# Kernel optimization log

Hardware: AMD Instinct MI355X
Metric: run time of the kernel (lower is better)

## Reference

```python
import jax, jax.numpy as jnp
import numpy as np

B, T, E, H = 2, 1024, 2048, 32
D = E // H
GROUP = (0.25, 0.25, 0.25, 0.25)
NEG = float(np.finfo(np.float32).min)


def quant_per_token(t, n_bits):
    # smoothquant-style: clamp(absmax, 1e-5) / qmax, per last-dim row
    qmax = 2 ** (n_bits - 1) - 1
    s = jnp.clip(jnp.abs(t).max(-1, keepdims=True), 1e-5, None) / qmax
    return jnp.round(t / s) * s


def w8a8_linear(x, W, b, quant_out=False):
    xq = quant_per_token(x, 8)           # per-token act quant
    Wq = quant_per_token(W, 8)           # per-output-channel weight quant (W: [out, in])
    y = xq @ Wq.T + b
    return quant_per_token(y, 8) if quant_out else y


def to_heads(x):
    # [B, T, E] -> [B*H, T, D]
    return x.reshape(B, T, H, D).transpose(0, 2, 1, 3).reshape(B * H, T, D)


def setup_inputs() -> dict:
    key = jax.random.key(0)
    ks = jax.random.split(key, 9)
    hidden_states = jax.random.normal(ks[0], (B, T, E), jnp.float32)
    causal = jnp.where(jnp.tril(jnp.ones((T, T), bool)), 0.0, NEG).astype(jnp.float32)
    attention_mask = jnp.broadcast_to(causal[None, None], (B, 1, T, T))
    w = 0.02
    return {
        'hidden_states': hidden_states,
        'attention_mask': attention_mask,
        'Wq': jax.random.normal(ks[1], (E, E), jnp.float32) * w,
        'bq': jax.random.normal(ks[2], (E,), jnp.float32) * w,
        'Wk': jax.random.normal(ks[3], (E, E), jnp.float32) * w,
        'bk': jax.random.normal(ks[4], (E,), jnp.float32) * w,
        'Wv': jax.random.normal(ks[5], (E, E), jnp.float32) * w,
        'bv': jax.random.normal(ks[6], (E,), jnp.float32) * w,
        'Wo': jax.random.normal(ks[7], (E, E), jnp.float32) * w,
        'bo': jax.random.normal(ks[8], (E,), jnp.float32) * w,
    }


def reference(hidden_states, attention_mask, Wq, bq, Wk, bk, Wv, bv, Wo, bo):
    scaling = D ** -0.5
    q = w8a8_linear(hidden_states, Wq, bq, quant_out=True) * scaling  # [B,T,E]
    k = w8a8_linear(hidden_states, Wk, bk)                            # [B,T,E]
    v = w8a8_linear(hidden_states, Wv, bv)                            # [B,T,E]

    # ---- heavy-hitter scoring pass (pre-4bit-quant K) ----
    q1, k1 = to_heads(q), to_heads(k)                                 # [BH,T,D]
    aw = jnp.einsum('btd,bsd->bts', q1, k1)                           # [BH,T,T]
    aw = aw.reshape(B, H, T, T) + attention_mask
    aw = jnp.maximum(aw, NEG).reshape(B * H, T, T)
    tmp_attn = jax.nn.softmax(aw, axis=-1)
    acc = tmp_attn.sum(axis=1).sum(axis=0)[None, :]                   # [1,T]
    row_vector = jnp.arange(T, 0, -1).astype(jnp.float32)[None, :]    # T, T-1, ..., 1
    acc = acc / row_vector / (B * H)

    # ---- group-wise top-k heavy-hitter selection ----
    range_size_or = int(T / len(GROUP) / 2)
    start = 1
    idx_list = []
    for i, ratio in enumerate(GROUP):
        rs = int(T * ratio)
        end = min(start + rs - 1, T) if i < len(GROUP) - 1 else T
        partial = acc[:, start - 1:end]
        _, ti = jax.lax.top_k(partial, range_size_or)
        idx_list.append(ti + start - 1)
        start = end + 1
    topk_idx = jnp.concatenate(idx_list, axis=-1).reshape(-1)

    # ---- mixed-precision K quantization ----
    k_abs = jnp.abs(k)
    # fake_quant_mix (8-bit): amax(...)[0] in torch indexes batch 0 -> scales [T,1]
    s_mix = jnp.clip(k_abs.max(-1, keepdims=True)[0] / 127.0, 1e-5, None)  # [T,1]
    k_imp = jnp.round(k / s_mix) * s_mix
    # fake_quant (4-bit, per-row): clamp then divide by 7
    s4 = jnp.clip(k_abs.max(-1, keepdims=True), 1e-5, None) / 7.0
    kq = jnp.round(k / s4) * s4
    kq = kq.at[:, topk_idx, :].set(k_imp[:, topk_idx, :])
    # fake_quant_v (4-bit, per-tensor)
    sv = jnp.clip(jnp.abs(v).max(), 1e-5, None) / 7.0
    vq = jnp.round(v / sv) * sv

    # ---- actual attention with quantized K/V ----
    q2, k2, v2 = to_heads(q), to_heads(kq), to_heads(vq)
    aw2 = jnp.einsum('btd,bsd->bts', q2, k2).reshape(B, H, T, T) + attention_mask
    aw2 = jnp.maximum(aw2, NEG).reshape(B * H, T, T)
    probs = jax.nn.softmax(aw2, axis=-1)
    out = jnp.einsum('bts,bsd->btd', probs, v2)                       # [BH,T,D]
    out = out.reshape(B, H, T, D).transpose(0, 2, 1, 3).reshape(B, T, E)
    return w8a8_linear(out, Wo, bo)
```

## Files before the change

kernel.cpp:

```cpp
#include <hip/hip_runtime.h>
#include <stdint.h>

#define NEG_INF (-__builtin_inff())
#define L2E 1.4426950408889634f

namespace {
constexpr int kT   = 1024;
constexpr int kE   = 2048;
}

using bf16x8 = __attribute__((ext_vector_type(8))) short;
using f32x4  = __attribute__((ext_vector_type(4))) float;
using i32x4  = __attribute__((ext_vector_type(4))) int;
using i32x16 = __attribute__((ext_vector_type(16))) int;

#define MFMA_BF16(a, b, c) __builtin_amdgcn_mfma_f32_16x16x32_bf16((a), (b), (c), 0, 0, 0)
#define MFMA_I8_32(a, b, c) __builtin_amdgcn_mfma_i32_32x32x32_i8((a), (b), (c), 0, 0, 0)

__device__ __forceinline__ void gload16(const void* g, void* l) {
  __builtin_amdgcn_global_load_lds((const __attribute__((address_space(1))) unsigned*)g,
                                   (__attribute__((address_space(3))) unsigned*)l, 16, 0, 0);
}
__device__ __forceinline__ unsigned bfr(float x) {
  unsigned u = __float_as_uint(x);
// ... 200 lines not shown
      q.z = (short)bfr(rintf(v.z / s));
      q.w = (short)bfr(rintf(v.w / s));
      *reinterpret_cast<short4*>(ki + (size_t)row * kE + i) = q;
    }
    if (tid == 0) skg[row] = s;
  } else {
    const int t = bid - 2048;
    const int tt = t & 15, bh = t >> 4;
    const int b = bh >> 5, h = bh & 31;
    const float sv = fmaxf(__uint_as_float(*vmax), 1e-5f) / 7.f;
    __shared__ short tr[64][80];
#pragma unroll
    for (int i = 0; i < 4; ++i) {
      const int e = i * 256 + tid;
      const int tok = e >> 4, d4 = (e & 15) * 4;
      const float4 v = *reinterpret_cast<const float4*>(
          &Vb[(size_t)(b * kT + tt * 64 + tok) * kE + h * 64 + d4]);
      tr[d4 + 0][tok] = (short)bfr(rintf(v.x / sv));
      tr[d4 + 1][tok] = (short)bfr(rintf(v.y / sv));
      tr[d4 + 2][tok] = (short)bfr(rintf(v.z / sv));
      tr[d4 + 3][tok] = (short)bfr(rintf(v.w / sv));
    }
    __syncthreads();
#pragma unroll
    for (int i = 0; i < 2; ++i) {
      const int e = i * 256 + tid;
      const int d = e >> 3, u = e & 7;
      const bf16x8 row = *reinterpret_cast<const bf16x8*>(&tr[d][u * 8]);
      *reinterpret_cast<bf16x8*>(&vt[(size_t)(bh * 64 + d) * kT + tt * 64 + u * 8]) = row;
    }
  }
}

__device__ __forceinline__ void gemm_i8_body(int m0, int n0,
                                             const int8_t* __restrict__ A,
                                             const float* __restrict__ sa,
                                             const int8_t* __restrict__ Bw,
                                             const float* __restrict__ sw,
                                             const float* __restrict__ bias,
                                             float* __restrict__ Y,
                                             int8_t* AsBase, int8_t* BsBase) {
  const int tid = threadIdx.x;
  const int lane = tid & 63, w = tid >> 6;
  const int l31 = lane & 31, lh = lane >> 5;
  const int wm = (w >> 1) * 64, wn = (w & 1) * 64;

  const i32x16 zero16 = {0};
  i32x16 acc00 = zero16, acc01 = zero16, acc10 = zero16, acc11 = zero16;

  auto stage = [&](int buf, int k0) {
    int8_t* As = AsBase + buf * 8192;
    int8_t* Bs = BsBase + buf * 8192;
#pragma unroll
    for (int i = 0; i < 2; ++i) {
      const int s = i * 256 + tid;
      const int row = s >> 2, gp = s & 3;
      const int gs = gp ^ ((row >> 1) & 3);
      gload16(A + (size_t)(m0 + row) * kE + k0 + gs * 16, As + s * 16);
    }
#pragma unroll
    for (int i = 0; i < 2; ++i) {
      const int s = i * 256 + tid;
      const int row = s >> 2, gp = s & 3;
      const int gs = gp ^ ((row >> 1) & 3);
      gload16(Bw + (size_t)(n0 + row) * kE + k0 + gs * 16, Bs + s * 16);
    }
  };

  stage(0, 0);
  __syncthreads();
  int cur = 0;

  const int ar0 = wm + l31, ar1 = wm + 32 + l31;
  const int br0 = wn + l31, br1 = wn + 32 + l31;
  const int sa0 = (ar0 >> 1) & 3, sa1 = (ar1 >> 1) & 3;
  const int sb0 = (br0 >> 1) & 3, sb1 = (br1 >> 1) & 3;

  for (int k0 = 0; k0 < kE; k0 += 64) {
    if (k0 + 64 < kE) stage(cur ^ 1, k0 + 64);
    const int8_t* As = AsBase + cur * 8192;
    const int8_t* Bs = BsBase + cur * 8192;
#pragma unroll
    for (int j = 0; j < 2; ++j) {
      const int gn = lh + 2 * j;
      const i32x4 a0 = *reinterpret_cast<const i32x4*>(As + ((ar0 << 2) + (gn ^ sa0)) * 16);
      const i32x4 a1 = *reinterpret_cast<const i32x4*>(As + ((ar1 << 2) + (gn ^ sa1)) * 16);
      const i32x4 b0 = *reinterpret_cast<const i32x4*>(Bs + ((br0 << 2) + (gn ^ sb0)) * 16);
      const i32x4 b1 = *reinterpret_cast<const i32x4*>(Bs + ((br1 << 2) + (gn ^ sb1)) * 16);
      acc00 = MFMA_I8_32(a0, b0, acc00);
      acc01 = MFMA_I8_32(a0, b1, acc01);
      acc10 = MFMA_I8_32(a1, b0, acc10);
      acc11 = MFMA_I8_32(a1, b1, acc11);
    }
    __syncthreads();
    cur ^= 1;
  }

#pragma unroll
  for (int fn = 0; fn < 2; ++fn) {
    const int col = n0 + wn + fn * 32 + l31;
    const float swn = sw[col], bn = bias[col];
#pragma unroll
    for (int fm = 0; fm < 2; ++fm) {
      const i32x16 accv = (fm == 0) ? ((fn == 0) ? acc00 : acc01)
                                    : ((fn == 0) ? acc10 : acc11);
      const int r0 = m0 + wm + fm * 32 + 4 * lh;
#pragma unroll
      for (int reg = 0; reg < 16; ++reg) {
        const int row = r0 + (reg & 3) + 8 * (reg >> 2);
        Y[(size_t)row * kE + col] = (float)accv[reg] * sa[row] * swn + bn;
      }
    }
  }
}

__global__ __launch_bounds__(256) void k_gemm_i8(const int8_t* __restrict__ A,
                                                 const float* __restrict__ sa,
                                                 const int8_t* __restrict__ Bw,
                                                 const float* __restrict__ sw,
                                                 const float* __restrict__ bias,
                                                 float* __restrict__ Y) {
  __shared__ int8_t As[2 * 8192];
  __shared__ int8_t Bs[2 * 8192];
  const int linear = blockIdx.x + (blockIdx.y << 4);
  const int nid = (linear & 7) * 32 + (linear >> 3);
  const int x = nid & 15, y = nid >> 4;
  gemm_i8_body(y * 128, x * 128, A, sa, Bw, sw, bias, Y, As, Bs);
}

__global__ __launch_bounds__(256) void k_gemm_qkv(const int8_t* __restrict__ A,
                                                  const float* __restrict__ sa,
                                                  const int8_t* __restrict__ Wq,
                                                  const int8_t* __restrict__ Wk,
                                                  const int8_t* __restrict__ Wv,
                                                  const float* __restrict__ sWall,
                                                  const float* __restrict__ bq,
                                                  const float* __restrict__ bk,
                                                  const float* __restrict__ bv,
                                                  float* __restrict__ qb,
                                                  float* __restrict__ kb,
                                                  float* __restrict__ vb) {
  __shared__ int8_t As[2 * 8192];
  __shared__ int8_t Bs[2 * 8192];
  const int linear = blockIdx.x + (blockIdx.y << 4) + (blockIdx.z << 8);
  const int nid = (linear & 7) * 96 + (linear >> 3);
  const int x = nid & 15, y = (nid >> 4) & 15, z = nid >> 8;
  const int8_t* Bw = (z == 0) ? Wq : (z == 1) ? Wk : Wv;
  const float* sw = sWall + (size_t)z * kE;
  const float* bias = (z == 0) ? bq : (z == 1) ? bk : bv;
  float* Y = (z == 0) ? qb : (z == 1) ? kb : vb;
  gemm_i8_body(y * 128, x * 128, A, sa, Bw, sw, bias, Y, As, Bs);
}

__global__ __launch_bounds__(256) void k_attn1(const short* __restrict__ qi,
                                               const short* __restrict__ khi,
                                               const short* __restrict__ klo,
                                               const float* __restrict__ sqg,
                                               float* __restrict__ accPart) {
  const int linear = blockIdx.x + (blockIdx.y << 3);
  const int nid = ((linear & 7) << 6) | (linear >> 3);
  const int r1 = nid & 7, r2 = 15 - r1, bh = nid >> 3;
  const int b = bh >> 5, h = bh & 31;
  const int tid = threadIdx.x, lane = tid & 63, w = tid >> 6;
  const int g = lane >> 4, c16 = lane & 15;
  const int swz = c16 & 7;

  __shared__ short qs1[64 * 64];
  __shared__ short qs2[64 * 64];
  __shared__ short hbuf[2][64 * 64];
  __shared__ short lbuf[2][64 * 64];
  __shared__ float accL[1024];
  __shared__ float Arow[128], Crow[128];

  for (int i = tid; i < 1024; i += 256) accL[i] = 0.f;

  const int st8 = tid >> 3, su = tid & 7;
  {
    const int tokb1 = b * kT + r1 * 64;
    const int tokb2 = b * kT + r2 * 64;
#pragma unroll
    for (int i = 0; i < 2; ++i) {
      const int tok = i * 32 + st8;
      const int co = ((su ^ (tok & 7)) << 3);
      gload16(qi + (size_t)(tokb1 + tok) * kE + h * 64 + co, &qs1[tok * 64 + su * 8]);
      gload16(qi + (size_t)(tokb2 + tok) * kE + h * 64 + co, &qs2[tok * 64 + su * 8]);
    }
  }
  auto stage = [&](int buf, int kt) {
    const int tokb = b * kT + kt * 64;
#pragma unroll
    for (int i = 0; i < 2; ++i) {
      const int tok = i * 32 + st8;
      const size_t gsrc = (size_t)(tokb + tok) * kE + h * 64 + ((su ^ (tok & 7)) << 3);
      gload16(khi + gsrc, &hbuf[buf][tok * 64 + su * 8]);
      gload16(klo + gsrc, &lbuf[buf][tok * 64 + su * 8]);
    }
  };

  stage(0, 0);
  __syncthreads();

  const int qrow = w * 16 + c16;
  const bf16x8 q1_0 = *reinterpret_cast<const bf16x8*>(&qs1[qrow * 64 + ((g ^ swz) << 3)]);
  const bf16x8 q1_1 = *reinterpret_cast<const bf16x8*>(&qs1[qrow * 64 + (((4 + g) ^ swz) << 3)]);
  const bf16x8 q2_0 = *reinterpret_cast<const bf16x8*>(&qs2[qrow * 64 + ((g ^ swz) << 3)]);
  const bf16x8 q2_1 = *reinterpret_cast<const bf16x8*>(&qs2[qrow * 64 + (((4 + g) ^ swz) << 3)]);
  const float A1c = sqg[b * kT + r1 * 64 + qrow] * L2E;
  const float A2c = sqg[b * kT + r2 * 64 + qrow] * L2E;

  float m1 = NEG_INF, l1 = 0.f, m2_ = NEG_INF, l2 = 0.f;
  int cur = 0;

  for (int kt = 0; kt <= r2; ++kt) {
    if (kt < r2) stage(cur ^ 1, kt + 1);
    const bool act1 = kt <= r1;
    float p1[4][4], p2[4][4];
    float pm1 = NEG_INF, pm2 = NEG_INF;
#pragma unroll
    for (int f = 0; f < 4; ++f) {
      const int tokl = f * 16 + c16;
      const bf16x8 ah0 = *reinterpret_cast<const bf16x8*>(&hbuf[cur][tokl * 64 + ((g ^ swz) << 3)]);
      const bf16x8 ah1 = *reinterpret_cast<const bf16x8*>(&hbuf[cur][tokl * 64 + (((4 + g) ^ swz) << 3)]);
      const bf16x8 al0 = *reinterpret_cast<const bf16x8*>(&lbuf[cur][tokl * 64 + ((g ^ swz) << 3)]);
      const bf16x8 al1 = *reinterpret_cast<const bf16x8*>(&lbuf[cur][tokl * 64 + (((4 + g) ^ swz) << 3)]);
      f32x4 sB = {0.f, 0.f, 0.f, 0.f};
      sB = MFMA_BF16(ah0, q2_0, sB);
      sB = MFMA_BF16(ah1, q2_1, sB);
      sB = MFMA_BF16(al0, q2_0, sB);
      sB = MFMA_BF16(al1, q2_1, sB);
      f32x4 sA = {0.f, 0.f, 0.f, 0.f};
      if (act1) {
        sA = MFMA_BF16(ah0, q1_0, sA);
        sA = MFMA_BF16(ah1, q1_1, sA);
        sA = MFMA_BF16(al0, q1_0, sA);
        sA = MFMA_BF16(al1, q1_1, sA);
      }
#pragma unroll
      for (int r = 0; r < 4; ++r) {
        const int tokd = f * 16 + g * 4 + r;
        float s2 = sB[r] * A2c;
        if (kt == r2 && tokd > qrow) s2 = NEG_INF;
        p2[f][r] = s2;
        pm2 = fmaxf(pm2, s2);
        float s1 = sA[r] * A1c;
        if (kt == r1 && tokd > qrow) s1 = NEG_INF;
        p1[f][r] = s1;
        pm1 = fmaxf(pm1, s1);
      }
    }
    {
      pm2 = fmaxf(pm2, __shfl_xor(pm2, 16));
      pm2 = fmaxf(pm2, __shfl_xor(pm2, 32));
      const bool upd = pm2 > m2_ + 8.f;
      const float mn = upd ? fmaxf(m2_, pm2) : m2_;
      const float fsc = fexp2(m2_ - mn);
      float rs = 0.f;
#pragma unroll
      for (int f = 0; f < 4; ++f)
#pragma unroll
        for (int r = 0; r < 4; ++r) rs += fexp2(p2[f][r] - mn);
      rs += __shfl_xor(rs, 16);
      rs += __shfl_xor(rs, 32);
      l2 = l2 * fsc + rs;
      m2_ = mn;
    }
    if (act1) {
      pm1 = fmaxf(pm1, __shfl_xor(pm1, 16));
      pm1 = fmaxf(pm1, __shfl_xor(pm1, 32));
      const bool upd = pm1 > m1 + 8.f;
      const float mn = upd ? fmaxf(m1, pm1) : m1;
      const float fsc = fexp2(m1 - mn);
      float rs = 0.f;
#pragma unroll
      for (int f = 0; f < 4; ++f)
#pragma unroll
        for (int r = 0; r < 4; ++r) rs += fexp2(p1[f][r] - mn);
      rs += __shfl_xor(rs, 16);
      rs += __shfl_xor(rs, 32);
      l1 = l1 * fsc + rs;
      m1 = mn;
    }
    __syncthreads();
    cur ^= 1;
  }

  if (g == 0) {
    Arow[qrow] = A1c;
    Crow[qrow] = -(m1 + __builtin_amdgcn_logf(l1));
    Arow[64 + qrow] = A2c;
    Crow[64 + qrow] = -(m2_ + __builtin_amdgcn_logf(l2));
  }
  stage(0, 0);
  __syncthreads();

  bf16x8 qa1_0[4], qa1_1[4], qa2_0[4], qa2_1[4];
  float Ar1[4][4], Cr1[4][4], Ar2[4][4], Cr2[4][4];
#pragma unroll
  for (int f = 0; f < 4; ++f) {
    const int qr = f * 16 + c16;
    qa1_0[f] = *reinterpret_cast<const bf16x8*>(&qs1[qr * 64 + ((g ^ swz) << 3)]);
    qa1_1[f] = *reinterpret_cast<const bf16x8*>(&qs1[qr * 64 + (((4 + g) ^ swz) << 3)]);
    qa2_0[f] = *reinterpret_cast<const bf16x8*>(&qs2[qr * 64 + ((g ^ swz) << 3)]);
    qa2_1[f] = *reinterpret_cast<const bf16x8*>(&qs2[qr * 64 + (((4 + g) ^ swz) << 3)]);
#pragma unroll
    for (int r = 0; r < 4; ++r) {
      const int tokd = f * 16 + g * 4 + r;
      Ar1[f][r] = Arow[tokd];
      Cr1[f][r] = Crow[tokd];
      Ar2[f][r] = Arow[64 + tokd];
      Cr2[f][r] = Crow[64 + tokd];
    }
  }

  const int ktokL = w * 16 + c16;
  cur = 0;
  for (int kt = 0; kt <= r2; ++kt) {
    if (kt < r2) stage(cur ^ 1, kt + 1);
    const bf16x8 kh0 = *reinterpret_cast<const bf16x8*>(&hbuf[cur][ktokL * 64 + ((g ^ swz) << 3)]);
    const bf16x8 kh1 = *reinterpret_cast<const bf16x8*>(&hbuf[cur][ktokL * 64 + (((4 + g) ^ swz) << 3)]);
    const bf16x8 kl0 = *reinterpret_cast<const bf16x8*>(&lbuf[cur][ktokL * 64 + ((g ^ swz) << 3)]);
    const bf16x8 kl1 = *reinterpret_cast<const bf16x8*>(&lbuf[cur][ktokL * 64 + (((4 + g) ^ swz) << 3)]);
    float csum = 0.f;
    if (kt < r2) {
#pragma unroll
      for (int f = 0; f < 4; ++f) {
        f32x4 sf = {0.f, 0.f, 0.f, 0.f};
        sf = MFMA_BF16(qa2_0[f], kh0, sf);
        sf = MFMA_BF16(qa2_1[f], kh1, sf);
        sf = MFMA_BF16(qa2_0[f], kl0, sf);
        sf = MFMA_BF16(qa2_1[f], kl1, sf);
#pragma unroll
        for (int r = 0; r < 4; ++r) csum += fexp2(fmaf(sf[r], Ar2[f][r], Cr2[f][r]));
      }
    } else {
#pragma unroll
      for (int f = 0; f < 4; ++f) {
        f32x4 sf = {0.f, 0.f, 0.f, 0.f};
        sf = MFMA_BF16(qa2_0[f], kh0, sf);
        sf = MFMA_BF16(qa2_1[f], kh1, sf);
        sf = MFMA_BF16(qa2_0[f], kl0, sf);
        sf = MFMA_BF16(qa2_1[f], kl1, sf);
#pragma unroll
        for (int r = 0; r < 4; ++r) {
          const float v = fexp2(fmaf(sf[r], Ar2[f][r], Cr2[f][r]));
          if (ktokL <= (f * 16 + g * 4 + r)) csum += v;
        }
      }
    }
    if (kt <= r1) {
      if (kt < r1) {
#pragma unroll
        for (int f = 0; f < 4; ++f) {
          f32x4 sf = {0.f, 0.f, 0.f, 0.f};
          sf = MFMA_BF16(qa1_0[f], kh0, sf);
          sf = MFMA_BF16(qa1_1[f], kh1, sf);
          sf = MFMA_BF16(qa1_0[f], kl0, sf);
          sf = MFMA_BF16(qa1_1[f], kl1, sf);
#pragma unroll
          for (int r = 0; r < 4; ++r) csum += fexp2(fmaf(sf[r], Ar1[f][r], Cr1[f][r]));
        }
      } else {
#pragma unroll
        for (int f = 0; f < 4; ++f) {
          f32x4 sf = {0.f, 0.f, 0.f, 0.f};
          sf = MFMA_BF16(qa1_0[f], kh0, sf);
          sf = MFMA_BF16(qa1_1[f], kh1, sf);
          sf = MFMA_BF16(qa1_0[f], kl0, sf);
          sf = MFMA_BF16(qa1_1[f], kl1, sf);
#pragma unroll
          for (int r = 0; r < 4; ++r) {
            const float v = fexp2(fmaf(sf[r], Ar1[f][r], Cr1[f][r]));
            if (ktokL <= (f * 16 + g * 4 + r)) csum += v;
          }
        }
      }
    }
    csum += __shfl_xor(csum, 16);
    csum += __shfl_xor(csum, 32);
    if (g == 0) accL[kt * 64 + ktokL] += csum;
    __syncthreads();
    cur ^= 1;
  }

  for (int i = tid; i < 1024; i += 256)
    accPart[(size_t)(bh * 8 + r1) * 1024 + i] = accL[i];
}

__global__ __launch_bounds__(1024) void k_acctopk(const float* __restrict__ part,
                                                  int* __restrict__ sel) {
  const int t = threadIdx.x;
  const int i = t & 255;
  const int sub = t >> 8;
  const int j = blockIdx.x * 256 + i;
  float s = 0.f;
  const int p0 = sub * 128;
  for (int p = p0; p < p0 + 128; ++p) s += part[(size_t)p * 1024 + j];
  __shared__ float partial[4][256];
  __shared__ float v[256];
  partial[sub][i] = s;
  __syncthreads();
  if (sub == 0) {
    const float tot = ((partial[0][i] + partial[1][i]) + partial[2][i]) + partial[3][i];
    v[i] = tot / (float)(kT - j) / 64.f;
  }
  __syncthreads();
  if (sub == 0) {
    const float vi = v[i];
    int rank = 0;
    for (int jj = 0; jj < 256; ++jj) {
      const float vj = v[jj];
      rank += (vj > vi) || (vj == vi && jj < i);
    }
    sel[j] = (rank < 128) ? 1 : 0;
  }
}

__global__ __launch_bounds__(256) void k_attn2(const short* __restrict__ qi,
                                               const short* __restrict__ ki,
                                               const short* __restrict__ vt,
                                               const float* __restrict__ sqg,
                                               const float* __restrict__ skg,
                                               const unsigned* __restrict__ vmax,
                                               float* __restrict__ ctx) {
  const int linear = blockIdx.x + (blockIdx.y << 3);
  const int nid = ((linear & 7) << 6) | (linear >> 3);
  const int r1 = nid & 7, r2 = 15 - r1, bh = nid >> 3;
  const int b = bh >> 5, h = bh & 31;
  const int tid = threadIdx.x, lane = tid & 63, w = tid >> 6;
  const int g = lane >> 4, c16 = lane & 15;
  const int swz = c16 & 7;
  const int wrow = w * 16 + c16;

  __shared__ short kbuf[2][64 * 64];
  __shared__ short vbuf[2][64 * 64];
  __shared__ float skl[2][64];

  const int qtokA = b * kT + r1 * 64 + wrow;
  const int qtokB = b * kT + r2 * 64 + wrow;
  bf16x8 qfA[2], qfB[2];
  qfA[0] = *reinterpret_cast<const bf16x8*>(qi + (size_t)qtokA * kE + h * 64 + g * 8);
  qfA[1] = *reinterpret_cast<const bf16x8*>(qi + (size_t)qtokA * kE + h * 64 + 32 + g * 8);
  qfB[0] = *reinterpret_cast<const bf16x8*>(qi + (size_t)qtokB * kE + h * 64 + g * 8);
  qfB[1] = *reinterpret_cast<const bf16x8*>(qi + (size_t)qtokB * kE + h * 64 + 32 + g * 8);
  const float sqA = sqg[qtokA] * L2E;
  const float sqB = sqg[qtokB] * L2E;
  const float sv = fmaxf(__uint_as_float(*vmax), 1e-5f) / 7.f;

  const int st8 = tid >> 3, su = tid & 7;
  auto stage = [&](int buf, int kt) {
    const int tokb = b * kT + kt * 64;
#pragma unroll
    for (int i = 0; i < 2; ++i) {
      const int tok = i * 32 + st8;
      gload16(ki + (size_t)(tokb + tok) * kE + h * 64 + ((su ^ (tok & 7)) << 3),
              &kbuf[buf][tok * 64 + su * 8]);
      gload16(vt + (size_t)(bh * 64 + tok) * kT + kt * 64 + ((su ^ (tok & 7)) << 3),
              &vbuf[buf][tok * 64 + su * 8]);
    }
    if (tid < 64) skl[buf][tid] = skg[tokb + tid];
  };

  float mA = NEG_INF, lA = 0.f, mB = NEG_INF, lB = 0.f;
  f32x4 otA[4], otB[4];
#pragma unroll
  for (int f = 0; f < 4; ++f) {
    otA[f] = (f32x4){0.f, 0.f, 0.f, 0.f};
    otB[f] = (f32x4){0.f, 0.f, 0.f, 0.f};
  }

  stage(0, 0);
  __syncthreads();
  int cur = 0;

  const int srcLo = c16 | ((g & 1) << 5);
  const int srcHi = srcLo | 16;
  const bool selq = ((g >> 1) & 1) != 0;

  for (int kt = 0; kt <= r2; ++kt) {
    if (kt < r2) stage(cur ^ 1, kt + 1);
    const bool act1 = kt <= r1;

    f32x4 sfB4[4], sfA4[4];
#pragma unroll
    for (int f = 0; f < 4; ++f) {
      const int tokl = f * 16 + c16;
      const bf16x8 k0 = *reinterpret_cast<const bf16x8*>(&kbuf[cur][tokl * 64 + ((g ^ swz) << 3)]);
      const bf16x8 k1 = *reinterpret_cast<const bf16x8*>(&kbuf[cur][tokl * 64 + (((4 + g) ^ swz) << 3)]);
      f32x4 s = {0.f, 0.f, 0.f, 0.f};
      s = MFMA_BF16(k0, qfB[0], s);
      s = MFMA_BF16(k1, qfB[1], s);
      sfB4[f] = s;
      f32x4 sa = {0.f, 0.f, 0.f, 0.f};
      if (act1) {
        sa = MFMA_BF16(k0, qfA[0], sa);
        sa = MFMA_BF16(k1, qfA[1], sa);
      }
      sfA4[f] = sa;
    }

    {
      float p[4][4];
      float pm = NEG_INF;
#pragma unroll
      for (int f = 0; f < 4; ++f)
#pragma unroll
        for (int r = 0; r < 4; ++r) {
          const int tokd = f * 16 + g * 4 + r;
          float s2 = sfB4[f][r] * skl[cur][tokd] * sqB;
          if (kt == r2 && tokd > wrow) s2 = NEG_INF;
          p[f][r] = s2;
          pm = fmaxf(pm, s2);
        }
      pm = fmaxf(pm, __shfl_xor(pm, 16));
      pm = fmaxf(pm, __shfl_xor(pm, 32));
      const bool upd = pm > mB + 8.f;
      const float mn = upd ? fmaxf(mB, pm) : mB;
      const float fsc = fexp2(mB - mn);
      mB = mn;
      float rs = 0.f;
#pragma unroll
      for (int f = 0; f < 4; ++f)
#pragma unroll
        for (int r = 0; r < 4; ++r) {
          const float e = fexp2(p[f][r] - mn);
          p[f][r] = e;
          rs += e;
        }
      rs += __shfl_xor(rs, 16);
      rs += __shfl_xor(rs, 32);
      lB = lB * fsc + rs;
      if (__any(upd)) {
#pragma unroll
        for (int f = 0; f < 4; ++f)
#pragma unroll
          for (int r = 0; r < 4; ++r) otB[f][r] *= fsc;
      }
#pragma unroll
      for (int c = 0; c < 2; ++c) {
        const unsigned q0a = pk2(p[2 * c][0], p[2 * c][1]);
        const unsigned q0b = pk2(p[2 * c][2], p[2 * c][3]);
        const unsigned q1a = pk2(p[2 * c + 1][0], p[2 * c + 1][1]);
        const unsigned q1b = pk2(p[2 * c + 1][2], p[2 * c + 1][3]);
        unsigned a0, a1;
        union { unsigned u[4]; bf16x8 v; } Bh;
        a0 = __shfl(q0a, srcLo); a1 = __shfl(q1a, srcLo); Bh.u[0] = selq ? a1 : a0;
        a0 = __shfl(q0b, srcLo); a1 = __shfl(q1b, srcLo); Bh.u[1] = selq ? a1 : a0;
        a0 = __shfl(q0a, srcHi); a1 = __shfl(q1a, srcHi); Bh.u[2] = selq ? a1 : a0;
        a0 = __shfl(q0b, srcHi); a1 = __shfl(q1b, srcHi); Bh.u[3] = selq ? a1 : a0;
#pragma unroll
        for (int fd = 0; fd < 4; ++fd) {
          const int d = fd * 16 + c16;
          const bf16x8 va = *reinterpret_cast<const bf16x8*>(
              &vbuf[cur][d * 64 + ((((c << 2) | g) ^ swz) << 3)]);
          otB[fd] = MFMA_BF16(va, Bh.v, otB[fd]);
        }
      }
    }

    if (act1) {
      float p[4][4];
      float pm = NEG_INF;
#pragma unroll
      for (int f = 0; f < 4; ++f)
#pragma unroll
        for (int r = 0; r < 4; ++r) {
          const int tokd = f * 16 + g * 4 + r;
          float s2 = sfA4[f][r] * skl[cur][tokd] * sqA;
          if (kt == r1 && tokd > wrow) s2 = NEG_INF;
          p[f][r] = s2;
          pm = fmaxf(pm, s2);
        }
      pm = fmaxf(pm, __shfl_xor(pm, 16));
      pm = fmaxf(pm, __shfl_xor(pm, 32));
      const bool upd = pm > mA + 8.f;
      const float mn = upd ? fmaxf(mA, pm) : mA;
      const float fsc = fexp2(mA - mn);
      mA = mn;
      float rs = 0.f;
#pragma unroll
      for (int f = 0; f < 4; ++f)
#pragma unroll
        for (int r = 0; r < 4; ++r) {
          const float e = fexp2(p[f][r] - mn);
          p[f][r] = e;
          rs += e;
        }
      rs += __shfl_xor(rs, 16);
      rs += __shfl_xor(rs, 32);
      lA = lA * fsc + rs;
      if (__any(upd)) {
#pragma unroll
        for (int f = 0; f < 4; ++f)
#pragma unroll
          for (int r = 0; r < 4; ++r) otA[f][r] *= fsc;
      }
#pragma unroll
      for (int c = 0; c < 2; ++c) {
        const unsigned q0a = pk2(p[2 * c][0], p[2 * c][1]);
        const unsigned q0b = pk2(p[2 * c][2], p[2 * c][3]);
        const unsigned q1a = pk2(p[2 * c + 1][0], p[2 * c + 1][1]);
        const unsigned q1b = pk2(p[2 * c + 1][2], p[2 * c + 1][3]);
        unsigned a0, a1;
        union { unsigned u[4]; bf16x8 v; } Bh;
        a0 = __shfl(q0a, srcLo); a1 = __shfl(q1a, srcLo); Bh.u[0] = selq ? a1 : a0;
        a0 = __shfl(q0b, srcLo); a1 = __shfl(q1b, srcLo); Bh.u[1] = selq ? a1 : a0;
        a0 = __shfl(q0a, srcHi); a1 = __shfl(q1a, srcHi); Bh.u[2] = selq ? a1 : a0;
        a0 = __shfl(q0b, srcHi); a1 = __shfl(q1b, srcHi); Bh.u[3] = selq ? a1 : a0;
#pragma unroll
        for (int fd = 0; fd < 4; ++fd) {
          const int d = fd * 16 + c16;
          const bf16x8 va = *reinterpret_cast<const bf16x8*>(
              &vbuf[cur][d * 64 + ((((c << 2) | g) ^ swz) << 3)]);
          otA[fd] = MFMA_BF16(va, Bh.v, otA[fd]);
        }
      }
    }

    __syncthreads();
    cur ^= 1;
  }

  const float ilA = sv / lA;
  const float ilB = sv / lB;
#pragma unroll
  for (int fd = 0; fd < 4; ++fd) {
    float4 oA, oB;
    oA.x = otA[fd][0] * ilA; oA.y = otA[fd][1] * ilA;
    oA.z = otA[fd][2] * ilA; oA.w = otA[fd][3] * ilA;
    oB.x = otB[fd][0] * ilB; oB.y = otB[fd][1] * ilB;
    oB.z = otB[fd][2] * ilB; oB.w = otB[fd][3] * ilB;
    *reinterpret_cast<float4*>(&ctx[(size_t)qtokA * kE + h * 64 + fd * 16 + g * 4]) = oA;
    *reinterpret_cast<float4*>(&ctx[(size_t)qtokB * kE + h * 64 + fd * 16 + g * 4]) = oB;
  }
}

extern "C" void kernel_launch(void* const* d_in, const int* in_sizes, int n_in,
                              void* d_out, int out_size, void* d_ws, size_t ws_size,
                              hipStream_t stream) {
  (void)in_sizes; (void)n_in; (void)out_size; (void)ws_size;
  const float* hs = (const float*)d_in[0];
  const float* Wq = (const float*)d_in[2];
  const float* bq = (const float*)d_in[3];
  const float* Wk = (const float*)d_in[4];
  const float* bk = (const float*)d_in[5];
  const float* Wv = (const float*)d_in[6];
  const float* bv = (const float*)d_in[7];
  const float* Wo = (const float*)d_in[8];
  const float* bo = (const float*)d_in[9];
  float* out = (float*)d_out;

  char* p = (char*)d_ws;
  auto take = [&](size_t bytes) {
    char* r = p;
    p += (bytes + 255) & ~(size_t)255;
    return r;
  };
  float* qb  = (float*)take((size_t)2048 * 2048 * 4);
  float* kb  = (float*)take((size_t)2048 * 2048 * 4);
  float* vb  = (float*)take((size_t)2048 * 2048 * 4);
  float* ctx = (float*)take((size_t)2048 * 2048 * 4);
  short* qiB = (short*)take((size_t)2048 * 2048 * 2);
  int8_t* xq  = (int8_t*)take((size_t)2048 * 2048);
  int8_t* woq = (int8_t*)take((size_t)2048 * 2048);
  float* sX    = (float*)take(2048 * 4);
  float* sWall = (float*)take(4 * 2048 * 4);
  float* sC    = (float*)take(2048 * 4);
  float* s4v   = (float*)take(2048 * 4);
  float* smix  = (float*)take(1024 * 4);
  int*   sel   = (int*)take(1024 * 4);
  float* sqg   = (float*)take(2048 * 4);
  float* skg   = (float*)take(2048 * 4);
  unsigned* vmax = (unsigned*)take(256);

  short* khi = (short*)qb;
  short* klo = (short*)qb + (size_t)2048 * 2048;
  short* kint = khi;
  short* vtp  = klo;
  float* accPart = ctx;
  int8_t* wqq = (int8_t*)ctx + ((size_t)2 << 20);
  int8_t* wkq = (int8_t*)ctx + ((size_t)6 << 20);
  int8_t* wvq = (int8_t*)ctx + ((size_t)10 << 20);
  int8_t* cq = xq;

  k_rowquant_all<<<dim3(2048, 5), 256, 0, stream>>>(hs, Wq, Wk, Wv, Wo,
                                                    xq, wqq, wkq, wvq, woq,
                                                    sX, sWall, vmax);

  k_gemm_qkv<<<dim3(16, 16, 3), 256, 0, stream>>>(xq, sX, wqq, wkq, wvq, sWall,
                                                  bq, bk, bv, qb, kb, vb);

  k_prep<<<2048, 256, 0, stream>>>(qb, kb, vb, qiB, sqg, khi, klo, s4v, smix, vmax);

  k_attn1<<<dim3(8, 64), 256, 0, stream>>>(qiB, khi, klo, sqg, accPart);
  k_acctopk<<<4, 1024, 0, stream>>>(accPart, sel);

  k_kvint<<<3072, 256, 0, stream>>>(kb, s4v, smix, sel, kint, skg, vb, vmax, vtp);

  k_attn2<<<dim3(8, 64), 256, 0, stream>>>(qiB, kint, vtp, sqg, skg, vmax, ctx);

  k_rowquant_i8<<<2048, 256, 0, stream>>>(ctx, cq, sC);
  k_gemm_i8<<<dim3(16, 16), 256, 0, stream>>>(cq, sC, woq, sWall + 3 * 2048, bo, out);
}
```

Before: 218.2 us.

## Split paired query tiles across separate waves in both attention kernels

Both attention kernels previously had each 4-wave block process two query tiles (r1 and r2) serially within the same waves. They now launch 512 threads, and waves 0-3 handle tile r1 while waves 4-7 handle tile r2, sharing the staged K/V buffers. Scoring-pass accumulators are kept per tile and summed at the end. This doubles in-flight wavefronts and shortens per-wave dependency chains. The cost is idle waves on the short tile once its range ends, plus higher register and LDS pressure per block.

Result: no change. 216.1 us (median of 3 runs) (-0.9%).

```diff
diff --git a/kernel.cpp b/kernel.cpp
--- a/kernel.cpp
+++ b/kernel.cpp
@@ -376,7 +376,7 @@
   gemm_i8_body(y * 128, x * 128, A, sa, Bw, sw, bias, Y, As, Bs);
 }
 
-__global__ __launch_bounds__(256) void k_attn1(const short* __restrict__ qi,
+__global__ __launch_bounds__(512) void k_attn1(const short* __restrict__ qi,
                                                const short* __restrict__ khi,
                                                const short* __restrict__ klo,
                                                const float* __restrict__ sqg,
@@ -388,226 +388,155 @@
   const int tid = threadIdx.x, lane = tid & 63, w = tid >> 6;
   const int g = lane >> 4, c16 = lane & 15;
   const int swz = c16 & 7;
-
-  __shared__ short qs1[64 * 64];
-  __shared__ short qs2[64 * 64];
+  const int myT = w >> 2, wl = w & 3;
+  const int myr = myT ? r2 : r1;
+
+  __shared__ short qs[2][64 * 64];
   __shared__ short hbuf[2][64 * 64];
   __shared__ short lbuf[2][64 * 64];
-  __shared__ float accL[1024];
+  __shared__ float accT[2][1024];
   __shared__ float Arow[128], Crow[128];
 
-  for (int i = tid; i < 1024; i += 256) accL[i] = 0.f;
+  for (int i = tid; i < 2048; i += 512) ((float*)accT)[i] = 0.f;
 
   const int st8 = tid >> 3, su = tid & 7;
   {
-    const int tokb1 = b * kT + r1 * 64;
-    const int tokb2 = b * kT + r2 * 64;
-#pragma unroll
-    for (int i = 0; i < 2; ++i) {
-      const int tok = i * 32 + st8;
-      const int co = ((su ^ (tok & 7)) << 3);
-      gload16(qi + (size_t)(tokb1 + tok) * kE + h * 64 + co, &qs1[tok * 64 + su * 8]);
-      gload16(qi + (size_t)(tokb2 + tok) * kE + h * 64 + co, &qs2[tok * 64 + su * 8]);
-    }
+    const int co = ((su ^ (st8 & 7)) << 3);
+    gload16(qi + (size_t)(b * kT + r1 * 64 + st8) * kE + h * 64 + co, &qs[0][st8 * 64 + su * 8]);
+    gload16(qi + (size_t)(b * kT + r2 * 64 + st8) * kE + h * 64 + co, &qs[1][st8 * 64 + su * 8]);
   }
   auto stage = [&](int buf, int kt) {
     const int tokb = b * kT + kt * 64;
-#pragma unroll
-    for (int i = 0; i < 2; ++i) {
-      const int tok = i * 32 + st8;
-      const size_t gsrc = (size_t)(tokb + tok) * kE + h * 64 + ((su ^ (tok & 7)) << 3);
-      gload16(khi + gsrc, &hbuf[buf][tok * 64 + su * 8]);
-      gload16(klo + gsrc, &lbuf[buf][tok * 64 + su * 8]);
-    }
+    const size_t gsrc = (size_t)(tokb + st8) * kE + h * 64 + ((su ^ (st8 & 7)) << 3);
+    gload16(khi + gsrc, &hbuf[buf][st8 * 64 + su * 8]);
+    gload16(klo + gsrc, &lbuf[buf][st8 * 64 + su * 8]);
   };
 
   stage(0, 0);
   __syncthreads();
 
-  const int qrow = w * 16 + c16;
-  const bf16x8 q1_0 = *reinterpret_cast<const bf16x8*>(&qs1[qrow * 64 + ((g ^ swz) << 3)]);
-  const bf16x8 q1_1 = *reinterpret_cast<const bf16x8*>(&qs1[qrow * 64 + (((4 + g) ^ swz) << 3)]);
-  const bf16x8 q2_0 = *reinterpret_cast<const bf16x8*>(&qs2[qrow * 64 + ((g ^ swz) << 3)]);
-  const bf16x8 q2_1 = *reinterpret_cast<const bf16x8*>(&qs2[qrow * 64 + (((4 + g) ^ swz) << 3)]);
-  const float A1c = sqg[b * kT + r1 * 64 + qrow] * L2E;
-  const float A2c = sqg[b * kT + r2 * 64 + qrow] * L2E;
-
-  float m1 = NEG_INF, l1 = 0.f, m2_ = NEG_INF, l2 = 0.f;
+  const int qrow = wl * 16 + c16;
+  const short* qsp = qs[myT];
+  const bf16x8 qf0 = *reinterpret_cast<const bf16x8*>(&qsp[qrow * 64 + ((g ^ swz) << 3)]);
+  const bf16x8 qf1 = *reinterpret_cast<const bf16x8*>(&qsp[qrow * 64 + (((4 + g) ^ swz) << 3)]);
+  const float Ac = sqg[b * kT + myr * 64 + qrow] * L2E;
+
+  float m = NEG_INF, l = 0.f;
   int cur = 0;
 
   for (int kt = 0; kt <= r2; ++kt) {
     if (kt < r2) stage(cur ^ 1, kt + 1);
-    const bool act1 = kt <= r1;
-    float p1[4][4], p2[4][4];
-    float pm1 = NEG_INF, pm2 = NEG_INF;
-#pragma unroll
-    for (int f = 0; f < 4; ++f) {
-      const int tokl = f * 16 + c16;
-      const bf16x8 ah0 = *reinterpret_cast<const bf16x8*>(&hbuf[cur][tokl * 64 + ((g ^ swz) << 3)]);
-      const bf16x8 ah1 = *reinterpret_cast<const bf16x8*>(&hbuf[cur][tokl * 64 + (((4 + g) ^ swz) << 3)]);
-      const bf16x8 al0 = *reinterpret_cast<const bf16x8*>(&lbuf[cur][tokl * 64 + ((g ^ swz) << 3)]);
-      const bf16x8 al1 = *reinterpret_cast<const bf16x8*>(&lbuf[cur][tokl * 64 + (((4 + g) ^ swz) << 3)]);
-      f32x4 sB = {0.f, 0.f, 0.f, 0.f};
-      sB = MFMA_BF16(ah0, q2_0, sB);
-      sB = MFMA_BF16(ah1, q2_1, sB);
-      sB = MFMA_BF16(al0, q2_0, sB);
-      sB = MFMA_BF16(al1, q2_1, sB);
-      f32x4 sA = {0.f, 0.f, 0.f, 0.f};
-      if (act1) {
-        sA = MFMA_BF16(ah0, q1_0, sA);
-        sA = MFMA_BF16(ah1, q1_1, sA);
-        sA = MFMA_BF16(al0, q1_0, sA);
-        sA = MFMA_BF16(al1, q1_1, sA);
+    if (kt <= myr) {
+      float p[4][4];
+      float pm = NEG_INF;
+#pragma unroll
+      for (int f = 0; f < 4; ++f) {
+        const int tokl = f * 16 + c16;
+        const bf16x8 ah0 = *reinterpret_cast<const bf16x8*>(&hbuf[cur][tokl * 64 + ((g ^ swz) << 3)]);
+        const bf16x8 ah1 = *reinterpret_cast<const bf16x8*>(&hbuf[cur][tokl * 64 + (((4 + g) ^ swz) << 3)]);
+        const bf16x8 al0 = *reinterpret_cast<const bf16x8*>(&lbuf[cur][tokl * 64 + ((g ^ swz) << 3)]);
+        const bf16x8 al1 = *reinterpret_cast<const bf16x8*>(&lbuf[cur][tokl * 64 + (((4 + g) ^ swz) << 3)]);
+        f32x4 sf = {0.f, 0.f, 0.f, 0.f};
+        sf = MFMA_BF16(ah0, qf0, sf);
+        sf = MFMA_BF16(ah1, qf1, sf);
+        sf = MFMA_BF16(al0, qf0, sf);
+        sf = MFMA_BF16(al1, qf1, sf);
+#pragma unroll
+        for (int r = 0; r < 4; ++r) {
+          const int tokd = f * 16 + g * 4 + r;
+          float s2 = sf[r] * Ac;
+          if (kt == myr && tokd > qrow) s2 = NEG_INF;
+          p[f][r] = s2;
+          pm = fmaxf(pm, s2);
+        }
       }
-#pragma unroll
-      for (int r = 0; r < 4; ++r) {
-        const int tokd = f * 16 + g * 4 + r;
-        float s2 = sB[r] * A2c;
-        if (kt == r2 && tokd > qrow) s2 = NEG_INF;
-        p2[f][r] = s2;
-        pm2 = fmaxf(pm2, s2);
-        float s1 = sA[r] * A1c;
-        if (kt == r1 && tokd > qrow) s1 = NEG_INF;
-        p1[f][r] = s1;
-        pm1 = fmaxf(pm1, s1);
-      }
-    }
-    {
-      pm2 = fmaxf(pm2, __shfl_xor(pm2, 16));
-      pm2 = fmaxf(pm2, __shfl_xor(pm2, 32));
-      const bool upd = pm2 > m2_ + 8.f;
-      const float mn = upd ? fmaxf(m2_, pm2) : m2_;
-      const float fsc = fexp2(m2_ - mn);
+      pm = fmaxf(pm, __shfl_xor(pm, 16));
+      pm = fmaxf(pm, __shfl_xor(pm, 32));
+      const bool upd = pm > m + 8.f;
+      const float mn = upd ? fmaxf(m, pm) : m;
+      const float fsc = fexp2(m - mn);
       float rs = 0.f;
 #pragma unroll
       for (int f = 0; f < 4; ++f)
 #pragma unroll
-        for (int r = 0; r < 4; ++r) rs += fexp2(p2[f][r] - mn);
+        for (int r = 0; r < 4; ++r) rs += fexp2(p[f][r] - mn);
       rs += __shfl_xor(rs, 16);
       rs += __shfl_xor(rs, 32);
-      l2 = l2 * fsc + rs;
-      m2_ = mn;
-    }
-    if (act1) {
-      pm1 = fmaxf(pm1, __shfl_xor(pm1, 16));
-      pm1 = fmaxf(pm1, __shfl_xor(pm1, 32));
-      const bool upd = pm1 > m1 + 8.f;
-      const float mn = upd ? fmaxf(m1, pm1) : m1;
-      const float fsc = fexp2(m1 - mn);
-      float rs = 0.f;
-#pragma unroll
-      for (int f = 0; f < 4; ++f)
-#pragma unroll
-        for (int r = 0; r < 4; ++r) rs += fexp2(p1[f][r] - mn);
-      rs += __shfl_xor(rs, 16);
-      rs += __shfl_xor(rs, 32);
-      l1 = l1 * fsc + rs;
-      m1 = mn;
+      l = l * fsc + rs;
+      m = mn;
     }
     __syncthreads();
     cur ^= 1;
   }
 
   if (g == 0) {
-    Arow[qrow] = A1c;
-    Crow[qrow] = -(m1 + __builtin_amdgcn_logf(l1));
-    Arow[64 + qrow] = A2c;
-    Crow[64 + qrow] = -(m2_ + __builtin_amdgcn_logf(l2));
+    Arow[myT * 64 + qrow] = Ac;
+    Crow[myT * 64 + qrow] = -(m + __builtin_amdgcn_logf(l));
   }
   stage(0, 0);
   __syncthreads();
 
-  bf16x8 qa1_0[4], qa1_1[4], qa2_0[4], qa2_1[4];
-  float Ar1[4][4], Cr1[4][4], Ar2[4][4], Cr2[4][4];
+  bf16x8 qa0[4], qa1[4];
+  float Ar[4][4], Cr[4][4];
 #pragma unroll
   for (int f = 0; f < 4; ++f) {
     const int qr = f * 16 + c16;
-    qa1_0[f] = *reinterpret_cast<const bf16x8*>(&qs1[qr * 64 + ((g ^ swz) << 3)]);
-    qa1_1[f] = *reinterpret_cast<const bf16x8*>(&qs1[qr * 64 + (((4 + g) ^ swz) << 3)]);
-    qa2_0[f] = *reinterpret_cast<const bf16x8*>(&qs2[qr * 64 + ((g ^ swz) << 3)]);
-    qa2_1[f] = *reinterpret_cast<const bf16x8*>(&qs2[qr * 64 + (((4 + g) ^ swz) << 3)]);
+    qa0[f] = *reinterpret_cast<const bf16x8*>(&qsp[qr * 64 + ((g ^ swz) << 3)]);
+    qa1[f] = *reinterpret_cast<const bf16x8*>(&qsp[qr * 64 + (((4 + g) ^ swz) << 3)]);
 #pragma unroll
     for (int r = 0; r < 4; ++r) {
-      const int tokd = f * 16 + g * 4 + r;
-      Ar1[f][r] = Arow[tokd];
-      Cr1[f][r] = Crow[tokd];
-      Ar2[f][r] = Arow[64 + tokd];
-      Cr2[f][r] = Crow[64 + tokd];
-    }
-  }
-
-  const int ktokL = w * 16 + c16;
+      const int tokd = myT * 64 + f * 16 + g * 4 + r;
+      Ar[f][r] = Arow[tokd];
+      Cr[f][r] = Crow[tokd];
+    }
+  }
+
+  const int ktokL = wl * 16 + c16;
   cur = 0;
   for (int kt = 0; kt <= r2; ++kt) {
     if (kt < r2) stage(cur ^ 1, kt + 1);
-    const bf16x8 kh0 = *reinterpret_cast<const bf16x8*>(&hbuf[cur][ktokL * 64 + ((g ^ swz) << 3)]);
-    const bf16x8 kh1 = *reinterpret_cast<const bf16x8*>(&hbuf[cur][ktokL * 64 + (((4 + g) ^ swz) << 3)]);
-    const bf16x8 kl0 = *reinterpret_cast<const bf16x8*>(&lbuf[cur][ktokL * 64 + ((g ^ swz) << 3)]);
-    const bf16x8 kl1 = *reinterpret_cast<const bf16x8*>(&lbuf[cur][ktokL * 64 + (((4 + g) ^ swz) << 3)]);
-    float csum = 0.f;
-    if (kt < r2) {
-#pragma unroll
-      for (int f = 0; f < 4; ++f) {
-        f32x4 sf = {0.f, 0.f, 0.f, 0.f};
-        sf = MFMA_BF16(qa2_0[f], kh0, sf);
-        sf = MFMA_BF16(qa2_1[f], kh1, sf);
-        sf = MFMA_BF16(qa2_0[f], kl0, sf);
-        sf = MFMA_BF16(qa2_1[f], kl1, sf);
-#pragma unroll
-        for (int r = 0; r < 4; ++r) csum += fexp2(fmaf(sf[r], Ar2[f][r], Cr2[f][r]));
-      }
-    } else {
-#pragma unroll
-      for (int f = 0; f < 4; ++f) {
-        f32x4 sf = {0.f, 0.f, 0.f, 0.f};
-        sf = MFMA_BF16(qa2_0[f], kh0, sf);
-        sf = MFMA_BF16(qa2_1[f], kh1, sf);
-        sf = MFMA_BF16(qa2_0[f], kl0, sf);
-        sf = MFMA_BF16(qa2_1[f], kl1, sf);
-#pragma unroll
-        for (int r = 0; r < 4; ++r) {
-          const float v = fexp2(fmaf(sf[r], Ar2[f][r], Cr2[f][r]));
-          if (ktokL <= (f * 16 + g * 4 + r)) csum += v;
-        }
-      }
-    }
-    if (kt <= r1) {
-      if (kt < r1) {
+    if (kt <= myr) {
+      const bf16x8 kh0 = *reinterpret_cast<const bf16x8*>(&hbuf[cur][ktokL * 64 + ((g ^ swz) << 3)]);
+      const bf16x8 kh1 = *reinterpret_cast<const bf16x8*>(&hbuf[cur][ktokL * 64 + (((4 + g) ^ swz) << 3)]);
+      const bf16x8 kl0 = *reinterpret_cast<const bf16x8*>(&lbuf[cur][ktokL * 64 + ((g ^ swz) << 3)]);
+      const bf16x8 kl1 = *reinterpret_cast<const bf16x8*>(&lbuf[cur][ktokL * 64 + (((4 + g) ^ swz) << 3)]);
+      float csum = 0.f;
+      if (kt < myr) {
 #pragma unroll
         for (int f = 0; f < 4; ++f) {
           f32x4 sf = {0.f, 0.f, 0.f, 0.f};
-          sf = MFMA_BF16(qa1_0[f], kh0, sf);
-          sf = MFMA_BF16(qa1_1[f], kh1, sf);
-          sf = MFMA_BF16(qa1_0[f], kl0, sf);
-          sf = MFMA_BF16(qa1_1[f], kl1, sf);
-#pragma unroll
-          for (int r = 0; r < 4; ++r) csum += fexp2(fmaf(sf[r], Ar1[f][r], Cr1[f][r]));
+          sf = MFMA_BF16(qa0[f], kh0, sf);
+          sf = MFMA_BF16(qa1[f], kh1, sf);
+          sf = MFMA_BF16(qa0[f], kl0, sf);
+          sf = MFMA_BF16(qa1[f], kl1, sf);
+#pragma unroll
+          for (int r = 0; r < 4; ++r) csum += fexp2(fmaf(sf[r], Ar[f][r], Cr[f][r]));
         }
       } else {
 #pragma unroll
         for (int f = 0; f < 4; ++f) {
           f32x4 sf = {0.f, 0.f, 0.f, 0.f};
-          sf = MFMA_BF16(qa1_0[f], kh0, sf);
-          sf = MFMA_BF16(qa1_1[f], kh1, sf);
-          sf = MFMA_BF16(qa1_0[f], kl0, sf);
-          sf = MFMA_BF16(qa1_1[f], kl1, sf);
+          sf = MFMA_BF16(qa0[f], kh0, sf);
+          sf = MFMA_BF16(qa1[f], kh1, sf);
+          sf = MFMA_BF16(qa0[f], kl0, sf);
+          sf = MFMA_BF16(qa1[f], kl1, sf);
 #pragma unroll
           for (int r = 0; r < 4; ++r) {
-            const float v = fexp2(fmaf(sf[r], Ar1[f][r], Cr1[f][r]));
+            const float v = fexp2(fmaf(sf[r], Ar[f][r], Cr[f][r]));
             if (ktokL <= (f * 16 + g * 4 + r)) csum += v;
           }
         }
       }
-    }
-    csum += __shfl_xor(csum, 16);
-    csum += __shfl_xor(csum, 32);
-    if (g == 0) accL[kt * 64 + ktokL] += csum;
+      csum += __shfl_xor(csum, 16);
+      csum += __shfl_xor(csum, 32);
+      if (g == 0) accT[myT][kt * 64 + ktokL] += csum;
+    }
     __syncthreads();
     cur ^= 1;
   }
 
-  for (int i = tid; i < 1024; i += 256)
-    accPart[(size_t)(bh * 8 + r1) * 1024 + i] = accL[i];
+  for (int i = tid; i < 1024; i += 512)
+    accPart[(size_t)(bh * 8 + r1) * 1024 + i] = accT[0][i] + accT[1][i];
 }
 
 __global__ __launch_bounds__(1024) void k_acctopk(const float* __restrict__ part,
@@ -639,7 +568,7 @@
   }
 }
 
-__global__ __launch_bounds__(256) void k_attn2(const short* __restrict__ qi,
+__global__ __launch_bounds__(512) void k_attn2(const short* __restrict__ qi,
                                                const short* __restrict__ ki,
                                                const short* __restrict__ vt,
                                                const float* __restrict__ sqg,
@@ -653,44 +582,35 @@
   const int tid = threadIdx.x, lane = tid & 63, w = tid >> 6;
   const int g = lane >> 4, c16 = lane & 15;
   const int swz = c16 & 7;
-  const int wrow = w * 16 + c16;
+  const int myT = w >> 2, wl = w & 3;
+  const int myr = myT ? r2 : r1;
+  const int wrow = wl * 16 + c16;
 
   __shared__ short kbuf[2][64 * 64];
   __shared__ short vbuf[2][64 * 64];
   __shared__ float skl[2][64];
 
-  const int qtokA = b * kT + r1 * 64 + wrow;
-  const int qtokB = b * kT + r2 * 64 + wrow;
-  bf16x8 qfA[2], qfB[2];
-  qfA[0] = *reinterpret_cast<const bf16x8*>(qi + (size_t)qtokA * kE + h * 64 + g * 8);
-  qfA[1] = *reinterpret_cast<const bf16x8*>(qi + (size_t)qtokA * kE + h * 64 + 32 + g * 8);
-  qfB[0] = *reinterpret_cast<const bf16x8*>(qi + (size_t)qtokB * kE + h * 64 + g * 8);
-  qfB[1] = *reinterpret_cast<const bf16x8*>(qi + (size_t)qtokB * kE + h * 64 + 32 + g * 8);
-  const float sqA = sqg[qtokA] * L2E;
-  const float sqB = sqg[qtokB] * L2E;
+  const int qtok = b * kT + myr * 64 + wrow;
+  bf16x8 qf[2];
+  qf[0] = *reinterpret_cast<const bf16x8*>(qi + (size_t)qtok * kE + h * 64 + g * 8);
+  qf[1] = *reinterpret_cast<const bf16x8*>(qi + (size_t)qtok * kE + h * 64 + 32 + g * 8);
+  const float sq2 = sqg[qtok] * L2E;
   const float sv = fmaxf(__uint_as_float(*vmax), 1e-5f) / 7.f;
 
   const int st8 = tid >> 3, su = tid & 7;
   auto stage = [&](int buf, int kt) {
     const int tokb = b * kT + kt * 64;
-#pragma unroll
-    for (int i = 0; i < 2; ++i) {
-      const int tok = i * 32 + st8;
-      gload16(ki + (size_t)(tokb + tok) * kE + h * 64 + ((su ^ (tok & 7)) << 3),
-              &kbuf[buf][tok * 64 + su * 8]);
-      gload16(vt + (size_t)(bh * 64 + tok) * kT + kt * 64 + ((su ^ (tok & 7)) << 3),
-              &vbuf[buf][tok * 64 + su * 8]);
-    }
+    gload16(ki + (size_t)(tokb + st8) * kE + h * 64 + ((su ^ (st8 & 7)) << 3),
+            &kbuf[buf][st8 * 64 + su * 8]);
+    gload16(vt + (size_t)(bh * 64 + st8) * kT + kt * 64 + ((su ^ (st8 & 7)) << 3),
+            &vbuf[buf][st8 * 64 + su * 8]);
     if (tid < 64) skl[buf][tid] = skg[tokb + tid];
   };
 
-  float mA = NEG_INF, lA = 0.f, mB = NEG_INF, lB = 0.f;
-  f32x4 otA[4], otB[4];
-#pragma unroll
-  for (int f = 0; f < 4; ++f) {
-    otA[f] = (f32x4){0.f, 0.f, 0.f, 0.f};
-    otB[f] = (f32x4){0.f, 0.f, 0.f, 0.f};
-  }
+  float m = NEG_INF, l = 0.f;
+  f32x4 ot[4];
+#pragma unroll
+  for (int f = 0; f < 4; ++f) ot[f] = (f32x4){0.f, 0.f, 0.f, 0.f};
 
   stage(0, 0);
   __syncthreads();
@@ -702,27 +622,19 @@
 
   for (int kt = 0; kt <= r2; ++kt) {
     if (kt < r2) stage(cur ^ 1, kt + 1);
-    const bool act1 = kt <= r1;
-
-    f32x4 sfB4[4], sfA4[4];
-#pragma unroll
-    for (int f = 0; f < 4; ++f) {
-      const int tokl = f * 16 + c16;
-      const bf16x8 k0 = *reinterpret_cast<const bf16x8*>(&kbuf[cur][tokl * 64 + ((g ^ swz) << 3)]);
-      const bf16x8 k1 = *reinterpret_cast<const bf16x8*>(&kbuf[cur][tokl * 64 + (((4 + g) ^ swz) << 3)]);
-      f32x4 s = {0.f, 0.f, 0.f, 0.f};
-      s = MFMA_BF16(k0, qfB[0], s);
-      s = MFMA_BF16(k1, qfB[1], s);
-      sfB4[f] = s;
-      f32x4 sa = {0.f, 0.f, 0.f, 0.f};
-      if (act1) {
-        sa = MFMA_BF16(k0, qfA[0], sa);
-        sa = MFMA_BF16(k1, qfA[1], sa);
+    if (kt <= myr) {
+      f32x4 sf4[4];
+#pragma unroll
+      for (int f = 0; f < 4; ++f) {
+        const int tokl = f * 16 + c16;
+        const bf16x8 k0 = *reinterpret_cast<const bf16x8*>(&kbuf[cur][tokl * 64 + ((g ^ swz) << 3)]);
+        const bf16x8 k1 = *reinterpret_cast<const bf16x8*>(&kbuf[cur][tokl * 64 + (((4 + g) ^ swz) << 3)]);
+        f32x4 s = {0.f, 0.f, 0.f, 0.f};
+        s = MFMA_BF16(k0, qf[0], s);
+        s = MFMA_BF16(k1, qf[1], s);
+        sf4[f] = s;
       }
-      sfA4[f] = sa;
-    }
-
-    {
+
       float p[4][4];
       float pm = NEG_INF;
 #pragma unroll
@@ -730,17 +642,17 @@
 #pragma unroll
         for (int r = 0; r < 4; ++r) {
           const int tokd = f * 16 + g * 4 + r;
-          float s2 = sfB4[f][r] * skl[cur][tokd] * sqB;
-          if (kt == r2 && tokd > wrow) s2 = NEG_INF;
+          float s2 = sf4[f][r] * skl[cur][tokd] * sq2;
+          if (kt == myr && tokd > wrow) s2 = NEG_INF;
           p[f][r] = s2;
           pm = fmaxf(pm, s2);
         }
       pm = fmaxf(pm, __shfl_xor(pm, 16));
       pm = fmaxf(pm, __shfl_xor(pm, 32));
-      const bool upd = pm > mB + 8.f;
-      const float mn = upd ? fmaxf(mB, pm) : mB;
-      const float fsc = fexp2(mB - mn);
-      mB = mn;
+      const bool upd = pm > m + 8.f;
+      const float mn = upd ? fmaxf(m, pm) : m;
+      const float fsc = fexp2(m - mn);
+      m = mn;
       float rs = 0.f;
 #pragma unroll
       for (int f = 0; f < 4; ++f)
@@ -752,12 +664,12 @@
         }
       rs += __shfl_xor(rs, 16);
       rs += __shfl_xor(rs, 32);
-      lB = lB * fsc + rs;
+      l = l * fsc + rs;
       if (__any(upd)) {
 #pragma unroll
         for (int f = 0; f < 4; ++f)
 #pragma unroll
-          for (int r = 0; r < 4; ++r) otB[f][r] *= fsc;
+          for (int r = 0; r < 4; ++r) ot[f][r] *= fsc;
       }
 #pragma unroll
       for (int c = 0; c < 2; ++c) {
@@ -776,85 +688,23 @@
           const int d = fd * 16 + c16;
           const bf16x8 va = *reinterpret_cast<const bf16x8*>(
               &vbuf[cur][d * 64 + ((((c << 2) | g) ^ swz) << 3)]);
-          otB[fd] = MFMA_BF16(va, Bh.v, otB[fd]);
+          ot[fd] = MFMA_BF16(va, Bh.v, ot[fd]);
         }
       }
     }
-
-    if (act1) {
-      float p[4][4];
-      float pm = NEG_INF;
-#pragma unroll
-      for (int f = 0; f < 4; ++f)
-#pragma unroll
-        for (int r = 0; r < 4; ++r) {
-          const int tokd = f * 16 + g * 4 + r;
-          float s2 = sfA4[f][r] * skl[cur][tokd] * sqA;
-          if (kt == r1 && tokd > wrow) s2 = NEG_INF;
-          p[f][r] = s2;
-          pm = fmaxf(pm, s2);
-        }
-      pm = fmaxf(pm, __shfl_xor(pm, 16));
-      pm = fmaxf(pm, __shfl_xor(pm, 32));
-      const bool upd = pm > mA + 8.f;
-      const float mn = upd ? fmaxf(mA, pm) : mA;
-      const float fsc = fexp2(mA - mn);
-      mA = mn;
-      float rs = 0.f;
-#pragma unroll
-      for (int f = 0; f < 4; ++f)
-#pragma unroll
-        for (int r = 0; r < 4; ++r) {
-          const float e = fexp2(p[f][r] - mn);
-          p[f][r] = e;
-          rs += e;
-        }
-      rs += __shfl_xor(rs, 16);
-      rs += __shfl_xor(rs, 32);
-      lA = lA * fsc + rs;
-      if (__any(upd)) {
-#pragma unroll
-        for (int f = 0; f < 4; ++f)
-#pragma unroll
-          for (int r = 0; r < 4; ++r) otA[f][r] *= fsc;
-      }
-#pragma unroll
-      for (int c = 0; c < 2; ++c) {
-        const unsigned q0a = pk2(p[2 * c][0], p[2 * c][1]);
-        const unsigned q0b = pk2(p[2 * c][2], p[2 * c][3]);
-        const unsigned q1a = pk2(p[2 * c + 1][0], p[2 * c + 1][1]);
-        const unsigned q1b = pk2(p[2 * c + 1][2], p[2 * c + 1][3]);
-        unsigned a0, a1;
-        union { unsigned u[4]; bf16x8 v; } Bh;
-        a0 = __shfl(q0a, srcLo); a1 = __shfl(q1a, srcLo); Bh.u[0] = selq ? a1 : a0;
-        a0 = __shfl(q0b, srcLo); a1 = __shfl(q1b, srcLo); Bh.u[1] = selq ? a1 : a0;
-        a0 = __shfl(q0a, srcHi); a1 = __shfl(q1a, srcHi); Bh.u[2] = selq ? a1 : a0;
-        a0 = __shfl(q0b, srcHi); a1 = __shfl(q1b, srcHi); Bh.u[3] = selq ? a1 : a0;
-#pragma unroll
-        for (int fd = 0; fd < 4; ++fd) {
-          const int d = fd * 16 + c16;
-          const bf16x8 va = *reinterpret_cast<const bf16x8*>(
-              &vbuf[cur][d * 64 + ((((c << 2) | g) ^ swz) << 3)]);
-          otA[fd] = MFMA_BF16(va, Bh.v, otA[fd]);
-        }
-      }
-    }
-
     __syncthreads();
     cur ^= 1;
   }
 
-  const float ilA = sv / lA;
-  const float ilB = sv / lB;
+  const float il = sv / l;
 #pragma unroll
   for (int fd = 0; fd < 4; ++fd) {
-    float4 oA, oB;
-    oA.x = otA[fd][0] * ilA; oA.y = otA[fd][1] * ilA;
-    oA.z = otA[fd][2] * ilA; oA.w = otA[fd][3] * ilA;
-    oB.x = otB[fd][0] * ilB; oB.y = otB[fd][1] * ilB;
-    oB.z = otB[fd][2] * ilB; oB.w = otB[fd][3] * ilB;
-    *reinterpret_cast<float4*>(&ctx[(size_t)qtokA * kE + h * 64 + fd * 16 + g * 4]) = oA;
-    *reinterpret_cast<float4*>(&ctx[(size_t)qtokB * kE + h * 64 + fd * 16 + g * 4]) = oB;
+    float4 o;
+    o.x = ot[fd][0] * il;
+    o.y = ot[fd][1] * il;
+    o.z = ot[fd][2] * il;
+    o.w = ot[fd][3] * il;
+    *reinterpret_cast<float4*>(&ctx[(size_t)qtok * kE + h * 64 + fd * 16 + g * 4]) = o;
   }
 }
 
@@ -915,12 +765,12 @@
 
   k_prep<<<2048, 256, 0, stream>>>(qb, kb, vb, qiB, sqg, khi, klo, s4v, smix, vmax);
 
-  k_attn1<<<dim3(8, 64), 256, 0, stream>>>(qiB, khi, klo, sqg, accPart);
+  k_attn1<<<dim3(8, 64), 512, 0, stream>>>(qiB, khi, klo, sqg, accPart);
   k_acctopk<<<4, 1024, 0, stream>>>(accPart, sel);
 
   k_kvint<<<3072, 256, 0, stream>>>(kb, s4v, smix, sel, kint, skg, vb, vmax, vtp);
 
-  k_attn2<<<dim3(8, 64), 256, 0, stream>>>(qiB, kint, vtp, sqg, skg, vmax, ctx);
+  k_attn2<<<dim3(8, 64), 512, 0, stream>>>(qiB, kint, vtp, sqg, skg, vmax, ctx);
 
   k_rowquant_i8<<<2048, 256, 0, stream>>>(ctx, cq, sC);
   k_gemm_i8<<<dim3(16, 16), 256, 0, stream>>>(cq, sC, woq, sWall + 3 * 2048, bo, out);
```
